# Kernel tuning notes

Measured on AMD Instinct MI355X. Metric: run time of the kernel, lower is better.

Reference implementation:

```python
import jax, jax.numpy as jnp
import numpy as np

EMBED_DIM = 128
HIDDEN_DIM = 32
BN_EPS = 1e-5


def setup_inputs() -> dict:
    key = jax.random.key(0)
    ks = jax.random.split(key, 11)
    B, N, D, H = 16, 2048, EMBED_DIM, HIDDEN_DIM
    s_d = 1.0 / np.sqrt(D)
    return {
        "f_in": jax.random.normal(ks[0], (B, N, D), dtype=jnp.float32),
        "w_q": jax.random.uniform(ks[1], (H, D), jnp.float32, -s_d, s_d),
        "b_q": jax.random.uniform(ks[2], (H,), jnp.float32, -s_d, s_d),
        "w_k": jax.random.uniform(ks[3], (H, D), jnp.float32, -s_d, s_d),
        "b_k": jax.random.uniform(ks[4], (H,), jnp.float32, -s_d, s_d),
        "w_v": jax.random.uniform(ks[5], (D, D), jnp.float32, -s_d, s_d),
        "b_v": jax.random.uniform(ks[6], (D,), jnp.float32, -s_d, s_d),
        "w_l": jax.random.uniform(ks[7], (D, D), jnp.float32, -s_d, s_d),
        "b_l": jax.random.uniform(ks[8], (D,), jnp.float32, -s_d, s_d),
        "bn_gamma": jnp.ones((D,), jnp.float32),
        "bn_beta": jnp.zeros((D,), jnp.float32),
    }


def reference(f_in, w_q, b_q, w_k, b_k, w_v, b_v, w_l, b_l, bn_gamma, bn_beta):
    # Q/K/V projections: (B, N, D) -> (B, N, h) / (B, N, D)
    q = jnp.einsum("bnd,hd->bnh", f_in, w_q) + b_q
    k = jnp.einsum("bnd,hd->bnh", f_in, w_k) + b_k
    v = jnp.einsum("bnd,ed->bne", f_in, w_v) + b_v
    # scores (B, N, N); softmax over dim=1 (query axis), then L1-renorm over keys
    a = jnp.einsum("bnh,bmh->bnm", q, k)
    a = jax.nn.softmax(a, axis=1)
    a = a / jnp.sum(a, axis=2, keepdims=True)
    f_sa = jnp.einsum("bnm,bme->bne", a, v)
    # LBR: Linear -> BatchNorm (training stats over B and N) -> ReLU, residual add
    x = f_in - f_sa
    y = jnp.einsum("bnd,ed->bne", x, w_l) + b_l
    mean = jnp.mean(y, axis=(0, 1))
    var = jnp.var(y, axis=(0, 1))  # biased, as BatchNorm uses for normalization
    y = bn_gamma * (y - mean) * jax.lax.rsqrt(var + BN_EPS) + bn_beta
    return jax.nn.relu(y) + f_sa
```

## Files before the change

kernel.cpp:

```cpp
#include <hip/hip_runtime.h>
#include <stdint.h>

#define NB 16
#define NN 2048
#define ND 128
#define NH 32
#define NS (NB*NN)
#define NT 32

typedef __attribute__((ext_vector_type(8))) short bf16x8;
typedef __attribute__((ext_vector_type(4))) float f32x4;

__device__ __forceinline__ unsigned short f2bf(float f){
  union { float f; unsigned int u; } v; v.f = f;
  unsigned int r = v.u + 0x7fffu + ((v.u >> 16) & 1u);
  return (unsigned short)(r >> 16);
}
__device__ __forceinline__ float bf2f(unsigned short u){
  union { unsigned int u; float f; } v; v.u = ((unsigned int)u) << 16;
  return v.f;
}
__device__ __forceinline__ float fexp2(float x){
  float r; asm("v_exp_f32 %0, %1" : "=v"(r) : "v"(x)); return r;
}

__global__ __launch_bounds__(256) void k_prep(const float* wq, const float* wk, const float* wv, const float* wl,
                                              unsigned short* oq, unsigned short* ok, unsigned short* ov, unsigned short* ol){
  int i = blockIdx.x*256 + threadIdx.x;
  if (i < 4096) oq[i] = f2bf(wq[i]);
  else if (i < 8192) ok[i-4096] = f2bf(wk[i-4096]);
  else if (i < 24576) ov[i-8192] = f2bf(wv[i-8192]);
  else if (i < 40960) ol[i-24576] = f2bf(wl[i-24576]);
}

__global__ __launch_bounds__(256) void k_qkv(const float* f, const unsigned short* wbq, const unsigned short* wbk,
                                             const unsigned short* wbv, const float* bq, const float* bk, const float* bv,
                                             unsigned short* Qb, unsigned short* Kb, unsigned short* Vb){
  int tid = threadIdx.x, wave = tid>>6, lane = tid&63, lr = lane&15, lg = lane>>4;
  long r0 = (long)blockIdx.x*64 + wave*16;
  bf16x8 a[4];
  const float* frow = f + (r0 + lr)*ND;
  #pragma unroll
  for (int ks=0; ks<4; ks++){
    const float* p = frow + ks*32 + lg*8;
    bf16x8 t;
    #pragma unroll
    for (int j=0;j<8;j++) t[j] = (short)f2bf(p[j]);
    a[ks] = t;
  }
  #pragma unroll
  for (int cs=0; cs<12; cs++){
    const unsigned short* wsrc; const float* bsrc; int cl;
    if (cs<2){ wsrc=wbq; bsrc=bq; cl=cs*16; }
    else if (cs<4){ wsrc=wbk; bsrc=bk; cl=(cs-2)*16; }
    else { wsrc=wbv; bsrc=bv; cl=(cs-4)*16; }
    f32x4 acc = {0.f,0.f,0.f,0.f};
    #pragma unroll
    for (int ks=0;ks<4;ks++){
      bf16x8 b = *(const bf16x8*)(wsrc + (cl+lr)*ND + ks*32 + lg*8);
      acc = __builtin_amdgcn_mfma_f32_16x16x32_bf16(a[ks], b, acc, 0, 0, 0);
    }
    float bias = bsrc[cl + lr];
    #pragma unroll
    for (int r=0;r<4;r++){
      float v = acc[r] + bias;
      if (cs<2) v *= 1.4426950408889634f;
      long row = r0 + lg*4 + r;
      if (cs<2) Qb[row*NH + cl+lr] = f2bf(v);
      else if (cs<4) Kb[row*NH + cl+lr] = f2bf(v);
      else Vb[row*ND + cl+lr] = f2bf(v);
    }
  }
}

__global__ __launch_bounds__(256) void k_csv(const unsigned short* Qb, const unsigned short* Kb,
                                             const unsigned short* Vb, unsigned short* VT){
  __shared__ unsigned short tr[128][65];
  __shared__ float wsh[64];
  int tid=threadIdx.x, wave=tid>>6, lane=tid&63, lr=lane&15, lg=lane>>4;
  int wg = (blockIdx.x & 7)*64 + (blockIdx.x >> 3);
  int b = wg >> 5;
  int m0 = (wg & 31)*64;
  const unsigned short* Qbb = Qb + (long)b*NN*NH;
  const unsigned short* Kbb = Kb + (long)b*NN*NH;
  const unsigned short* Vbb = Vb + ((long)b*NN + m0)*ND;
  bf16x8 vreg[4];
  #pragma unroll
  for (int it=0; it<4; it++){
    int i = it*256 + tid;
    int r = i >> 4, c8 = (i & 15)*8;
    vreg[it] = *(const bf16x8*)(Vbb + r*ND + c8);
  }
  bf16x8 kf = *(const bf16x8*)(Kbb + (m0 + wave*16 + lr)*NH + lg*8);
  float csum = 0.f;
  for (int n0=0; n0<NN; n0+=64){
    #pragma unroll
    for (int u=0; u<4; u++){
      bf16x8 qf = *(const bf16x8*)(Qbb + (n0+u*16+lr)*NH + lg*8);
      f32x4 c = {0.f,0.f,0.f,0.f};
      c = __builtin_amdgcn_mfma_f32_16x16x32_bf16(qf, kf, c, 0, 0, 0);
      csum += fexp2(c[0]) + fexp2(c[1]) + fexp2(c[2]) + fexp2(c[3]);
    }
  }
  csum += __shfl_xor(csum, 16, 64);
  csum += __shfl_xor(csum, 32, 64);
  #pragma unroll
  for (int it=0; it<4; it++){
    int i = it*256 + tid;
    int r = i >> 4, c8 = (i & 15)*8;
    #pragma unroll
    for (int j=0;j<8;j++) tr[c8+j][r] = (unsigned short)vreg[it][j];
  }
  if (lg == 0) wsh[wave*16 + lr] = 1.f / csum;
  __syncthreads();
  unsigned short* VTb = VT + (long)b*144*NN;
  #pragma unroll
  for (int it=0; it<9; it++){
    int i = it*256 + tid;
    int e = i >> 4, m4 = (i & 15)*4;
    ushort4 o;
    if (e < 128){
      o.x = f2bf(bf2f(tr[e][m4+0]) * wsh[m4+0]);
      o.y = f2bf(bf2f(tr[e][m4+1]) * wsh[m4+1]);
      o.z = f2bf(bf2f(tr[e][m4+2]) * wsh[m4+2]);
      o.w = f2bf(bf2f(tr[e][m4+3]) * wsh[m4+3]);
    } else if (e == 128){
      o.x = f2bf(wsh[m4+0]); o.y = f2bf(wsh[m4+1]);
      o.z = f2bf(wsh[m4+2]); o.w = f2bf(wsh[m4+3]);
    } else { o.x = o.y = o.z = o.w = 0; }
    *(ushort4*)(VTb + (long)e*NN + m0 + m4) = o;
  }
}

__global__ __launch_bounds__(256) void k_pv(const unsigned short* Qb, const unsigned short* Kb,
                                            const unsigned short* VT, float* fsa){
  __shared__ __align__(16) unsigned char vbuf[3][20480];
  __shared__ __align__(16) unsigned char kbuf[2][4096];
  __shared__ __align__(16) unsigned char es[4][2048];
  int tid=threadIdx.x, wave=tid>>6, lane=tid&63, lr=lane&15, lg=lane>>4;
  int wg = (blockIdx.x & 7)*64 + (blockIdx.x >> 3);
  int b = wg >> 5;
  int nloc = (wg & 31)*64 + wave*16;
  const unsigned short* Qbb = Qb + (long)b*NN*NH;
  const unsigned short* Kbb = Kb + (long)b*NN*NH;
  const unsigned short* VTb = VT + (long)b*144*NN;

  int vrow_lo = lane>>3;
  int vblk    = lane&7;
  int krow_lo = lane>>2;
  int kblk    = lane&3;

  auto stageV = [&](int buf, int m0c){
    #pragma unroll
    for (int t=0;t<5;t++){
      int i = wave*5 + t;
      int e = i*8 + vrow_lo;
      int sblk = vblk ^ (e&7);
      __builtin_amdgcn_global_load_lds(
        (const __attribute__((address_space(1))) unsigned int*)(VTb + (long)e*NN + m0c + sblk*8),
        (__attribute__((address_space(3))) unsigned int*)(&vbuf[buf][i*1024]), 16, 0, 0);
    }
  };
  auto stageK = [&](int buf, int m0c){
    int r = wave*16 + krow_lo;
    int sblk = kblk ^ ((krow_lo>>1)&3);
    __builtin_amdgcn_global_load_lds(
      (const __attribute__((address_space(1))) unsigned int*)(Kbb + (long)(m0c + r)*NH + sblk*8),
      (__attribute__((address_space(3))) unsigned int*)(&kbuf[buf][wave*1024]), 16, 0, 0);
  };

  bf16x8 qf = *(const bf16x8*)(Qbb + (nloc+lr)*NH + lg*8);
  f32x4 acc[9];
  #pragma unroll
  for (int cs=0;cs<9;cs++) acc[cs] = (f32x4){0.f,0.f,0.f,0.f};

  stageV(0, 0);
  stageK(0, 0);
  stageV(1, 64);

  int vc = 0, kc = 0, vn2 = 2;
  for (int it = 0; it < NT; ++it){
    int m0 = it<<6;
    if (it < NT-1) asm volatile("s_waitcnt vmcnt(5)" ::: "memory");
    else           asm volatile("s_waitcnt vmcnt(0)" ::: "memory");
    __builtin_amdgcn_s_barrier();
    if (it+1 < NT) stageK(kc^1, m0+64);
    if (it+2 < NT) stageV(vn2, m0+128);
    #pragma unroll
    for (int s=0;s<4;s++){
      bf16x8 kf = *(const bf16x8*)(&kbuf[kc][(s*16+lr)*64 + ((lg ^ ((lr>>1)&3))<<4)]);
      f32x4 c = {0.f,0.f,0.f,0.f};
      c = __builtin_amdgcn_mfma_f32_16x16x32_bf16(qf, kf, c, 0, 0, 0);
      #pragma unroll
      for (int r=0;r<4;r++){
        int row = lg*4 + r, col = s*16 + lr;
        *(unsigned short*)(&es[wave][(row<<7) + ((col*2) ^ ((row&7)<<4))]) = f2bf(fexp2(c[r]));
      }
    }
    __builtin_amdgcn_s_setprio(1);
    #pragma unroll
    for (int ks=0; ks<2; ks++){
      bf16x8 ea = *(const bf16x8*)(&es[wave][(lr<<7) + ((ks*64 + (lg<<4)) ^ ((lr&7)<<4))]);
      #pragma unroll
      for (int cs=0; cs<9; cs++){
        int e = cs*16 + lr;
        bf16x8 vb = *(const bf16x8*)(&vbuf[vc][(e<<7) + ((ks*64 + (lg<<4)) ^ ((e&7)<<4))]);
        acc[cs] = __builtin_amdgcn_mfma_f32_16x16x32_bf16(ea, vb, acc[cs], 0, 0, 0);
      }
    }
    __builtin_amdgcn_s_setprio(0);
    vc = (vc==2)?0:vc+1;
    vn2 = (vn2==2)?0:vn2+1;
    kc ^= 1;
  }
  long grow0 = (long)b*NN + nloc;
  #pragma unroll
  for (int r=0;r<4;r++){
    float den = __shfl(acc[8][r], lane & 48, 64);
    float rinv = 1.f / den;
    int row = lg*4 + r;
    #pragma unroll
    for (int cs=0;cs<8;cs++)
      fsa[(grow0 + row)*ND + cs*16 + lr] = acc[cs][r] * rinv;
  }
}

__global__ __launch_bounds__(256) void k_lin(const float* f, const float* fsa, const unsigned short* wbl, const float* bl,
                                             unsigned short* ybuf, float* part){
  __shared__ float psum[4][128], psq[4][128];
  int tid=threadIdx.x, wave=tid>>6, lane=tid&63, lr=lane&15, lg=lane>>4;
  long r0 = (long)blockIdx.x*64 + wave*16;
  bf16x8 a[4];
  {
    const float* fr = f + (r0+lr)*ND;
    const float* sr = fsa + (r0+lr)*ND;
    #pragma unroll
    for (int ks=0;ks<4;ks++){
      bf16x8 t;
      #pragma unroll
      for (int j=0;j<8;j++){
        int d = ks*32 + lg*8 + j;
        t[j] = (short)f2bf(fr[d] - sr[d]);
      }
      a[ks] = t;
    }
  }
  #pragma unroll
  for (int cs=0;cs<8;cs++){
    f32x4 acc = {0.f,0.f,0.f,0.f};
    #pragma unroll
    for (int ks=0;ks<4;ks++){
      bf16x8 bfr = *(const bf16x8*)(wbl + (cs*16+lr)*ND + ks*32 + lg*8);
      acc = __builtin_amdgcn_mfma_f32_16x16x32_bf16(a[ks], bfr, acc, 0, 0, 0);
    }
    float bias = bl[cs*16+lr];
    float l1=0.f, l2=0.f;
    #pragma unroll
    for (int r=0;r<4;r++){
      float y = acc[r] + bias;
      ybuf[(r0 + lg*4 + r)*ND + cs*16 + lr] = f2bf(y);
      l1 += y; l2 += y*y;
    }
    l1 += __shfl_xor(l1,16,64); l1 += __shfl_xor(l1,32,64);
    l2 += __shfl_xor(l2,16,64); l2 += __shfl_xor(l2,32,64);
    if (lg==0){ psum[wave][cs*16+lr] = l1; psq[wave][cs*16+lr] = l2; }
  }
  __syncthreads();
  if (tid < 128){
    float t1 = psum[0][tid]+psum[1][tid]+psum[2][tid]+psum[3][tid];
    float t2 = psq[0][tid]+psq[1][tid]+psq[2][tid]+psq[3][tid];
    part[tid*512 + blockIdx.x] = t1;
    part[65536 + tid*512 + blockIdx.x] = t2;
  }
}

__global__ __launch_bounds__(64) void k_bnred(const float* part, const float* gamma, const float* beta, float* bnstat){
  int c = blockIdx.x, t = threadIdx.x;
  float s=0.f, q=0.f;
  for (int i=t; i<512; i+=64){ s += part[c*512+i]; q += part[65536 + c*512+i]; }
  #pragma unroll
  for (int m=1; m<64; m<<=1){ s += __shfl_xor(s,m,64); q += __shfl_xor(q,m,64); }
  if (t==0){
    float mean = s * (1.f/(float)NS);
    float var  = q * (1.f/(float)NS) - mean*mean;
    float rstd = rsqrtf(var + 1e-5f);
    float sc = gamma[c]*rstd;
    bnstat[c] = sc;
    bnstat[128+c] = beta[c] - mean*sc;
  }
}

__global__ __launch_bounds__(256) void k_final(const unsigned short* ybuf, const float* fsa, const float* bnstat,
                                               float* out){
  long i0 = ((long)blockIdx.x*256 + threadIdx.x)*8;
  int c0 = (int)(i0 & (ND-1));
  bf16x8 yv = *(const bf16x8*)(ybuf + i0);
  f32x4 f0 = *(const f32x4*)(fsa + i0);
  f32x4 f1 = *(const f32x4*)(fsa + i0 + 4);
  f32x4 o0, o1;
  #pragma unroll
  for (int j=0;j<8;j++){
    int c = c0 + j;
    float v = bf2f((unsigned short)yv[j]) * bnstat[c] + bnstat[128+c];
    v = v > 0.f ? v : 0.f;
    float add = (j<4) ? f0[j] : f1[j-4];
    if (j<4) o0[j] = v + add; else o1[j-4] = v + add;
  }
  *(f32x4*)(out + i0) = o0;
  *(f32x4*)(out + i0 + 4) = o1;
}

extern "C" void kernel_launch(void* const* d_in, const int* in_sizes, int n_in,
                              void* d_out, int out_size, void* d_ws, size_t ws_size,
                              hipStream_t stream){
  const float* f_in  = (const float*)d_in[0];
  const float* w_q   = (const float*)d_in[1];
  const float* b_q   = (const float*)d_in[2];
  const float* w_k   = (const float*)d_in[3];
  const float* b_k   = (const float*)d_in[4];
  const float* w_v   = (const float*)d_in[5];
  const float* b_v   = (const float*)d_in[6];
  const float* w_l   = (const float*)d_in[7];
  const float* b_l   = (const float*)d_in[8];
  const float* gamma = (const float*)d_in[9];
  const float* beta  = (const float*)d_in[10];
  float* out = (float*)d_out;
  char* ws = (char*)d_ws;

  unsigned short* wbq = (unsigned short*)(ws + 0);
  unsigned short* wbk = (unsigned short*)(ws + 8192);
  unsigned short* wbv = (unsigned short*)(ws + 16384);
  unsigned short* wbl = (unsigned short*)(ws + 49152);
  unsigned short* Qb  = (unsigned short*)(ws + 81920);
  unsigned short* Kb  = (unsigned short*)(ws + 2179072);
  unsigned short* Vb  = (unsigned short*)(ws + 4276224);
  unsigned short* VT  = (unsigned short*)(ws + 12795904);
  float*          fsa = (float*)(ws + 22233088);
  unsigned short* ybuf= (unsigned short*)(ws + 39010304);
  float*          part= (float*)(ws + 47398912);
  float*          bnst= (float*)(ws + 47923200);

  k_prep  <<<160, 256, 0, stream>>>(w_q, w_k, w_v, w_l, wbq, wbk, wbv, wbl);
  k_qkv   <<<512, 256, 0, stream>>>(f_in, wbq, wbk, wbv, b_q, b_k, b_v, Qb, Kb, Vb);
  k_csv   <<<512, 256, 0, stream>>>(Qb, Kb, Vb, VT);
  k_pv    <<<512, 256, 0, stream>>>(Qb, Kb, VT, fsa);
  k_lin   <<<512, 256, 0, stream>>>(f_in, fsa, wbl, b_l, ybuf, part);
  k_bnred <<<128, 64, 0, stream>>>(part, gamma, beta, bnst);
  k_final <<<2048,256, 0, stream>>>(ybuf, fsa, bnst, out);
}
```

Measured before the change: 125.9 us.

## Rework attention PV kernel to 32x32 MFMA with register-resident scores and bf16 fsa

The k_pv kernel moves from 16x16x32 to 32x32x16 bf16 MFMA tiles, with 2 waves of 32 query rows each. K fragments are loaded directly into registers instead of staged through LDS. The exp scores are packed and swapped across lanes so they feed the PV MFMA without an LDS round-trip. VT is padded to 160 rows to fit the 32-wide tiles, and the f_sa intermediate is stored as bf16 to halve its traffic in k_lin and k_final. This lowers precision of f_sa in the residual add and halves the waves per block, so it relies on per-wave efficiency to hide latency.

```diff
diff --git a/kernel.cpp b/kernel.cpp
--- a/kernel.cpp
+++ b/kernel.cpp
@@ -10,6 +10,7 @@
 
 typedef __attribute__((ext_vector_type(8))) short bf16x8;
 typedef __attribute__((ext_vector_type(4))) float f32x4;
+typedef __attribute__((ext_vector_type(16))) float f32x16;
 
 __device__ __forceinline__ unsigned short f2bf(float f){
   union { float f; unsigned int u; } v; v.f = f;
@@ -113,7 +114,7 @@
   }
   if (lg == 0) wsh[wave*16 + lr] = 1.f / csum;
   __syncthreads();
-  unsigned short* VTb = VT + (long)b*144*NN;
+  unsigned short* VTb = VT + (long)b*160*NN;
   #pragma unroll
   for (int it=0; it<9; it++){
     int i = it*256 + tid;
@@ -130,102 +131,126 @@
     } else { o.x = o.y = o.z = o.w = 0; }
     *(ushort4*)(VTb + (long)e*NN + m0 + m4) = o;
   }
-}
-
-__global__ __launch_bounds__(256) void k_pv(const unsigned short* Qb, const unsigned short* Kb,
-                                            const unsigned short* VT, float* fsa){
-  __shared__ __align__(16) unsigned char vbuf[3][20480];
-  __shared__ __align__(16) unsigned char kbuf[2][4096];
-  __shared__ __align__(16) unsigned char es[4][2048];
-  int tid=threadIdx.x, wave=tid>>6, lane=tid&63, lr=lane&15, lg=lane>>4;
+  {
+    int e = 144 + (tid >> 4), m4 = (tid & 15)*4;
+    ushort4 z; z.x = z.y = z.z = z.w = 0;
+    *(ushort4*)(VTb + (long)e*NN + m0 + m4) = z;
+  }
+}
+
+__global__ __launch_bounds__(128) void k_pv(const unsigned short* Qb, const unsigned short* Kb,
+                                            const unsigned short* VT, unsigned short* fsab){
+  __shared__ __align__(16) unsigned char vts[3][20480];
+  int tid=threadIdx.x, wave=tid>>6, lane=tid&63;
+  int l31 = lane & 31, H = lane >> 5;
   int wg = (blockIdx.x & 7)*64 + (blockIdx.x >> 3);
   int b = wg >> 5;
-  int nloc = (wg & 31)*64 + wave*16;
+  int q0 = (wg & 31)*64 + wave*32;
   const unsigned short* Qbb = Qb + (long)b*NN*NH;
   const unsigned short* Kbb = Kb + (long)b*NN*NH;
-  const unsigned short* VTb = VT + (long)b*144*NN;
-
-  int vrow_lo = lane>>3;
-  int vblk    = lane&7;
-  int krow_lo = lane>>2;
-  int kblk    = lane&3;
+  const unsigned short* VTb = VT + (long)b*160*NN;
 
   auto stageV = [&](int buf, int m0c){
     #pragma unroll
-    for (int t=0;t<5;t++){
-      int i = wave*5 + t;
-      int e = i*8 + vrow_lo;
-      int sblk = vblk ^ (e&7);
+    for (int t=0;t<10;t++){
+      int i = wave*10 + t;
+      int e = i*8 + (lane>>3);
+      int sblk = (lane&7) ^ (e&7);
       __builtin_amdgcn_global_load_lds(
         (const __attribute__((address_space(1))) unsigned int*)(VTb + (long)e*NN + m0c + sblk*8),
-        (__attribute__((address_space(3))) unsigned int*)(&vbuf[buf][i*1024]), 16, 0, 0);
+        (__attribute__((address_space(3))) unsigned int*)(&vts[buf][i*1024]), 16, 0, 0);
     }
   };
-  auto stageK = [&](int buf, int m0c){
-    int r = wave*16 + krow_lo;
-    int sblk = kblk ^ ((krow_lo>>1)&3);
-    __builtin_amdgcn_global_load_lds(
-      (const __attribute__((address_space(1))) unsigned int*)(Kbb + (long)(m0c + r)*NH + sblk*8),
-      (__attribute__((address_space(3))) unsigned int*)(&kbuf[buf][wave*1024]), 16, 0, 0);
-  };
-
-  bf16x8 qf = *(const bf16x8*)(Qbb + (nloc+lr)*NH + lg*8);
-  f32x4 acc[9];
-  #pragma unroll
-  for (int cs=0;cs<9;cs++) acc[cs] = (f32x4){0.f,0.f,0.f,0.f};
-
+
+  bf16x8 qf0 = *(const bf16x8*)(Qbb + (long)(q0 + l31)*NH + 8*H);
+  bf16x8 qf1 = *(const bf16x8*)(Qbb + (long)(q0 + l31)*NH + 16 + 8*H);
+  asm volatile("" ::: "memory");
+  bf16x8 k00 = *(const bf16x8*)(Kbb + (long)(l31)*NH + 8*H);
+  bf16x8 k01 = *(const bf16x8*)(Kbb + (long)(l31)*NH + 16 + 8*H);
+  bf16x8 k10 = *(const bf16x8*)(Kbb + (long)(32 + l31)*NH + 8*H);
+  bf16x8 k11 = *(const bf16x8*)(Kbb + (long)(32 + l31)*NH + 16 + 8*H);
+  asm volatile("" ::: "memory");
   stageV(0, 0);
-  stageK(0, 0);
   stageV(1, 64);
 
-  int vc = 0, kc = 0, vn2 = 2;
+  f32x16 acc[5];
+  #pragma unroll
+  for (int c=0;c<5;c++)
+    #pragma unroll
+    for (int r=0;r<16;r++) acc[c][r] = 0.f;
+
+  union U { unsigned int u[4]; bf16x8 v; };
+
+  int vc = 0, vs = 2;
   for (int it = 0; it < NT; ++it){
-    int m0 = it<<6;
-    if (it < NT-1) asm volatile("s_waitcnt vmcnt(5)" ::: "memory");
-    else           asm volatile("s_waitcnt vmcnt(0)" ::: "memory");
+    if (it == 0)         asm volatile("s_waitcnt vmcnt(10)" ::: "memory");
+    else if (it == 1)    asm volatile("s_waitcnt vmcnt(14)" ::: "memory");
+    else if (it == NT-1) asm volatile("s_waitcnt vmcnt(8)"  ::: "memory");
+    else                 asm volatile("s_waitcnt vmcnt(18)" ::: "memory");
     __builtin_amdgcn_s_barrier();
-    if (it+1 < NT) stageK(kc^1, m0+64);
-    if (it+2 < NT) stageV(vn2, m0+128);
-    #pragma unroll
-    for (int s=0;s<4;s++){
-      bf16x8 kf = *(const bf16x8*)(&kbuf[kc][(s*16+lr)*64 + ((lg ^ ((lr>>1)&3))<<4)]);
-      f32x4 c = {0.f,0.f,0.f,0.f};
-      c = __builtin_amdgcn_mfma_f32_16x16x32_bf16(qf, kf, c, 0, 0, 0);
-      #pragma unroll
-      for (int r=0;r<4;r++){
-        int row = lg*4 + r, col = s*16 + lr;
-        *(unsigned short*)(&es[wave][(row<<7) + ((col*2) ^ ((row&7)<<4))]) = f2bf(fexp2(c[r]));
+    if (it + 2 < NT) stageV(vs, (it+2)*64);
+    asm volatile("" ::: "memory");
+    const unsigned char* vcur = &vts[vc][0];
+
+    #pragma unroll
+    for (int t=0;t<2;t++){
+      f32x16 s;
+      #pragma unroll
+      for (int r=0;r<16;r++) s[r] = 0.f;
+      s = __builtin_amdgcn_mfma_f32_32x32x16_bf16(t ? k10 : k00, qf0, s, 0, 0, 0);
+      s = __builtin_amdgcn_mfma_f32_32x32x16_bf16(t ? k11 : k01, qf1, s, 0, 0, 0);
+      #pragma unroll
+      for (int r=0;r<16;r++) s[r] = fexp2(s[r]);
+      unsigned int pk[8], sw[8];
+      #pragma unroll
+      for (int p=0;p<8;p++){
+        asm("v_cvt_pk_bf16_f32 %0, %1, %2" : "=v"(pk[p]) : "v"(s[2*p]), "v"(s[2*p+1]));
+        sw[p] = (unsigned int)__shfl_xor((int)pk[p], 32, 64);
       }
-    }
-    __builtin_amdgcn_s_setprio(1);
-    #pragma unroll
-    for (int ks=0; ks<2; ks++){
-      bf16x8 ea = *(const bf16x8*)(&es[wave][(lr<<7) + ((ks*64 + (lg<<4)) ^ ((lr&7)<<4))]);
-      #pragma unroll
-      for (int cs=0; cs<9; cs++){
-        int e = cs*16 + lr;
-        bf16x8 vb = *(const bf16x8*)(&vbuf[vc][(e<<7) + ((ks*64 + (lg<<4)) ^ ((e&7)<<4))]);
-        acc[cs] = __builtin_amdgcn_mfma_f32_16x16x32_bf16(ea, vb, acc[cs], 0, 0, 0);
+      bool h0 = (H == 0);
+      U fa0, fa1;
+      fa0.u[0] = h0 ? pk[0] : sw[2];  fa0.u[1] = h0 ? pk[1] : sw[3];
+      fa0.u[2] = h0 ? sw[0] : pk[2];  fa0.u[3] = h0 ? sw[1] : pk[3];
+      fa1.u[0] = h0 ? pk[4] : sw[6];  fa1.u[1] = h0 ? pk[5] : sw[7];
+      fa1.u[2] = h0 ? sw[4] : pk[6];  fa1.u[3] = h0 ? sw[5] : pk[7];
+      __builtin_amdgcn_s_setprio(1);
+      #pragma unroll
+      for (int ksl=0; ksl<2; ksl++){
+        int KS = 2*t + ksl;
+        const U& fa = ksl ? fa1 : fa0;
+        #pragma unroll
+        for (int c=0;c<5;c++){
+          int e = c*32 + l31;
+          bf16x8 vb = *(const bf16x8*)(vcur + (e<<7) + (((2*KS + H) ^ (e&7))<<4));
+          acc[c] = __builtin_amdgcn_mfma_f32_32x32x16_bf16(fa.v, vb, acc[c], 0, 0, 0);
+        }
       }
-    }
-    __builtin_amdgcn_s_setprio(0);
+      __builtin_amdgcn_s_setprio(0);
+    }
+    if (it + 1 < NT){
+      long mb = (long)(it+1)*64;
+      k00 = *(const bf16x8*)(Kbb + (mb + l31)*NH + 8*H);
+      k01 = *(const bf16x8*)(Kbb + (mb + l31)*NH + 16 + 8*H);
+      k10 = *(const bf16x8*)(Kbb + (mb + 32 + l31)*NH + 8*H);
+      k11 = *(const bf16x8*)(Kbb + (mb + 32 + l31)*NH + 16 + 8*H);
+    }
     vc = (vc==2)?0:vc+1;
-    vn2 = (vn2==2)?0:vn2+1;
-    kc ^= 1;
-  }
-  long grow0 = (long)b*NN + nloc;
-  #pragma unroll
-  for (int r=0;r<4;r++){
-    float den = __shfl(acc[8][r], lane & 48, 64);
+    vs = (vs==2)?0:vs+1;
+  }
+  long rowbase = (long)b*NN + q0;
+  #pragma unroll
+  for (int r=0;r<16;r++){
+    float den = __shfl(acc[4][r], lane & 32, 64);
     float rinv = 1.f / den;
-    int row = lg*4 + r;
-    #pragma unroll
-    for (int cs=0;cs<8;cs++)
-      fsa[(grow0 + row)*ND + cs*16 + lr] = acc[cs][r] * rinv;
-  }
-}
-
-__global__ __launch_bounds__(256) void k_lin(const float* f, const float* fsa, const unsigned short* wbl, const float* bl,
+    int rho = (r&3) + 8*(r>>2) + 4*H;
+    long row = rowbase + rho;
+    #pragma unroll
+    for (int c=0;c<4;c++)
+      fsab[row*ND + c*32 + l31] = f2bf(acc[c][r] * rinv);
+  }
+}
+
+__global__ __launch_bounds__(256) void k_lin(const float* f, const unsigned short* fsab, const unsigned short* wbl, const float* bl,
                                              unsigned short* ybuf, float* part){
   __shared__ float psum[4][128], psq[4][128];
   int tid=threadIdx.x, wave=tid>>6, lane=tid&63, lr=lane&15, lg=lane>>4;
@@ -233,14 +258,15 @@
   bf16x8 a[4];
   {
     const float* fr = f + (r0+lr)*ND;
-    const float* sr = fsa + (r0+lr)*ND;
+    const unsigned short* sr = fsab + (r0+lr)*ND;
     #pragma unroll
     for (int ks=0;ks<4;ks++){
+      bf16x8 sv = *(const bf16x8*)(sr + ks*32 + lg*8);
       bf16x8 t;
       #pragma unroll
       for (int j=0;j<8;j++){
         int d = ks*32 + lg*8 + j;
-        t[j] = (short)f2bf(fr[d] - sr[d]);
+        t[j] = (short)f2bf(fr[d] - bf2f((unsigned short)sv[j]));
       }
       a[ks] = t;
     }
@@ -290,21 +316,20 @@
   }
 }
 
-__global__ __launch_bounds__(256) void k_final(const unsigned short* ybuf, const float* fsa, const float* bnstat,
+__global__ __launch_bounds__(256) void k_final(const unsigned short* ybuf, const unsigned short* fsab, const float* bnstat,
                                                float* out){
   long i0 = ((long)blockIdx.x*256 + threadIdx.x)*8;
   int c0 = (int)(i0 & (ND-1));
   bf16x8 yv = *(const bf16x8*)(ybuf + i0);
-  f32x4 f0 = *(const f32x4*)(fsa + i0);
-  f32x4 f1 = *(const f32x4*)(fsa + i0 + 4);
+  bf16x8 fv = *(const bf16x8*)(fsab + i0);
   f32x4 o0, o1;
   #pragma unroll
   for (int j=0;j<8;j++){
     int c = c0 + j;
     float v = bf2f((unsigned short)yv[j]) * bnstat[c] + bnstat[128+c];
     v = v > 0.f ? v : 0.f;
-    float add = (j<4) ? f0[j] : f1[j-4];
-    if (j<4) o0[j] = v + add; else o1[j-4] = v + add;
+    float r = v + bf2f((unsigned short)fv[j]);
+    if (j<4) o0[j] = r; else o1[j-4] = r;
   }
   *(f32x4*)(out + i0) = o0;
   *(f32x4*)(out + i0 + 4) = o1;
@@ -335,7 +360,7 @@
   unsigned short* Kb  = (unsigned short*)(ws + 2179072);
   unsigned short* Vb  = (unsigned short*)(ws + 4276224);
   unsigned short* VT  = (unsigned short*)(ws + 12795904);
-  float*          fsa = (float*)(ws + 22233088);
+  unsigned short* fsab= (unsigned short*)(ws + 23281664);
   unsigned short* ybuf= (unsigned short*)(ws + 39010304);
   float*          part= (float*)(ws + 47398912);
   float*          bnst= (float*)(ws + 47923200);
@@ -343,8 +368,8 @@
   k_prep  <<<160, 256, 0, stream>>>(w_q, w_k, w_v, w_l, wbq, wbk, wbv, wbl);
   k_qkv   <<<512, 256, 0, stream>>>(f_in, wbq, wbk, wbv, b_q, b_k, b_v, Qb, Kb, Vb);
   k_csv   <<<512, 256, 0, stream>>>(Qb, Kb, Vb, VT);
-  k_pv    <<<512, 256, 0, stream>>>(Qb, Kb, VT, fsa);
-  k_lin   <<<512, 256, 0, stream>>>(f_in, fsa, wbl, b_l, ybuf, part);
+  k_pv    <<<512, 128, 0, stream>>>(Qb, Kb, VT, fsab);
+  k_lin   <<<512, 256, 0, stream>>>(f_in, fsab, wbl, b_l, ybuf, part);
   k_bnred <<<128, 64, 0, stream>>>(part, gamma, beta, bnst);
-  k_final <<<2048,256, 0, stream>>>(ybuf, fsa, bnst, out);
-}
+  k_final <<<2048,256, 0, stream>>>(ybuf, fsab, bnst, out);
+}
```

Result: slower. 132.5 us (+5.2%).
